# Kernel tuning notes

Hardware: AMD Instinct MI355X
Metric: run time of the kernel (lower is better)

## Reference

```python
import jax, jax.numpy as jnp
import numpy as np

EPSILON = 1e-4
MAX_ITER = 10


def setup_inputs() -> dict:
    key = jax.random.key(0)
    k1, k2, k3 = jax.random.split(key, 3)
    B, N, M = 64, 1024, 1024
    s = jax.random.uniform(k1, (B, N, M), dtype=jnp.float32)
    nrows = jax.random.randint(k2, (B,), 0, N, dtype=jnp.int32)
    ncols = jax.random.randint(k3, (B,), 0, M, dtype=jnp.int32)
    return {"s": s, "nrows": nrows, "ncols": ncols}


def reference(s, nrows, ncols):
    # s: [B, N, M]; nrows/ncols: [B] valid row/col counts per sample.
    B, N, M = s.shape
    row_mask = jnp.arange(N, dtype=nrows.dtype)[None, :] < nrows[:, None]  # [B, N]
    col_mask = jnp.arange(M, dtype=ncols.dtype)[None, :] < ncols[:, None]  # [B, M]
    mask = row_mask[:, :, None] & col_mask[:, None, :]  # [B, N, M]

    s = s + EPSILON
    for i in range(MAX_ITER):
        # i even -> column normalization (sum over dim 1); i odd -> row normalization (sum over dim 2)
        axis = 2 if i % 2 == 1 else 1
        ssum = jnp.sum(s, axis=axis, keepdims=True)
        tmp = jnp.where(mask, 1.0 / ssum, jnp.zeros((), dtype=s.dtype))
        s = s * tmp
    return s
```

## Files before the change

kernel.cpp:

```cpp
#include <hip/hip_runtime.h>

#define EPS 1e-4f

constexpr int Bn = 64;
constexpr int Nn = 1024;
constexpr int Mn = 1024;
constexpr int NSPLIT = 16;
constexpr int CHUNK  = Nn / NSPLIT;
constexpr int SLOT0  = 2 * NSPLIT;
constexpr int SLOT1  = 64;

__device__ __forceinline__ unsigned pk2(float a, float b) {
    unsigned ua = __float_as_uint(a); ua = (ua + 0x7fffu + ((ua >> 16) & 1u)) >> 16;
    unsigned ub = __float_as_uint(b); ub = (ub + 0x7fffu + ((ub >> 16) & 1u)) >> 16;
    return ua | (ub << 16);
}
__device__ __forceinline__ float lo16(unsigned v) { return __uint_as_float(v << 16); }
__device__ __forceinline__ float hi16(unsigned v) { return __uint_as_float(v & 0xffff0000u); }

__global__ __launch_bounds__(256) void fuse0_kernel(
        const float* __restrict__ s, unsigned short* __restrict__ sc,
        float* __restrict__ p) {
    const int b = blockIdx.x, sp = blockIdx.y;
    const int t = threadIdx.x, half = t >> 7, tc = t & 127;
    float acc[8];
    #pragma unroll
    for (int k = 0; k < 8; ++k) acc[k] = 0.f;
    for (int j = 0; j < CHUNK; j += 2) {
        const int n = sp * CHUNK + j + half;
        const size_t roff = ((size_t)b * Nn + n) * Mn;
        const float4* src = reinterpret_cast<const float4*>(s + roff) + 2 * tc;
        float4 v0 = src[0], v1 = src[1];
        v0.x += EPS; v0.y += EPS; v0.z += EPS; v0.w += EPS;
        v1.x += EPS; v1.y += EPS; v1.z += EPS; v1.w += EPS;
        acc[0] += v0.x; acc[1] += v0.y; acc[2] += v0.z; acc[3] += v0.w;
        acc[4] += v1.x; acc[5] += v1.y; acc[6] += v1.z; acc[7] += v1.w;
        uint4 w = { pk2(v0.x, v0.y), pk2(v0.z, v0.w),
                    pk2(v1.x, v1.y), pk2(v1.z, v1.w) };
        reinterpret_cast<uint4*>(sc + roff)[tc] = w;
    }
    float* pp = p + ((size_t)(b * SLOT1 + sp * 2 + half)) * Mn + tc * 8;
    float4 o0 = {acc[0], acc[1], acc[2], acc[3]};
    float4 o1 = {acc[4], acc[5], acc[6], acc[7]};
    *reinterpret_cast<float4*>(pp)     = o0;
    *reinterpret_cast<float4*>(pp + 4) = o1;
}

__global__ __launch_bounds__(256) void col_final_kernel(
        const float* __restrict__ p, const int* __restrict__ ncols,
        float* __restrict__ c, int slots) {
    const int b = blockIdx.x;
    const int m0 = threadIdx.x << 2;
    float sx = 0.f, sy = 0.f, sz = 0.f, sw = 0.f;
    for (int k = 0; k < slots; ++k) {
        float4 v = *reinterpret_cast<const float4*>(
            p + ((size_t)(b * SLOT1 + k)) * Mn + m0);
        sx += v.x; sy += v.y; sz += v.z; sw += v.w;
    }
    const int nc = ncols[b];
    float4 o;
    o.x = (m0 + 0 < nc && sx > 0.f) ? 1.f / sx : 0.f;
    o.y = (m0 + 1 < nc && sy > 0.f) ? 1.f / sy : 0.f;
    o.z = (m0 + 2 < nc && sz > 0.f) ? 1.f / sz : 0.f;
    o.w = (m0 + 3 < nc && sw > 0.f) ? 1.f / sw : 0.f;
    *reinterpret_cast<float4*>(c + (size_t)b * Mn + m0) = o;
}

__global__ __launch_bounds__(256) void rowcol_kernel(
        const unsigned short* __restrict__ sc, const float* __restrict__ c,
        const int* __restrict__ nrows, float* __restrict__ p) {
    const int b = blockIdx.x;
    const int t = threadIdx.x, w = t >> 6, l = t & 63;
    const int n0 = blockIdx.y * 64 + w * 16;
    const float4* cb = reinterpret_cast<const float4*>(c + (size_t)b * Mn);
    const float4 c0 = cb[2 * l], c1 = cb[2 * l + 1];
    const float4 c2 = cb[128 + 2 * l], c3 = cb[128 + 2 * l + 1];
    const int nr = nrows[b];
    float acc[16];
    #pragma unroll
    for (int k = 0; k < 16; ++k) acc[k] = 0.f;
    for (int j = 0; j < 16; ++j) {
        const int n = n0 + j;
        const uint4* row = reinterpret_cast<const uint4*>(sc + ((size_t)b * Nn + n) * Mn);
        uint4 a = row[l], d = row[64 + l];
        const float v0 = lo16(a.x), v1 = hi16(a.x), v2 = lo16(a.y), v3 = hi16(a.y);
        const float v4 = lo16(a.z), v5 = hi16(a.z), v6 = lo16(a.w), v7 = hi16(a.w);
        const float v8 = lo16(d.x), v9 = hi16(d.x), v10 = lo16(d.y), v11 = hi16(d.y);
        const float v12 = lo16(d.z), v13 = hi16(d.z), v14 = lo16(d.w), v15 = hi16(d.w);
        float part = v0 * c0.x + v1 * c0.y + v2 * c0.z + v3 * c0.w
                   + v4 * c1.x + v5 * c1.y + v6 * c1.z + v7 * c1.w
                   + v8 * c2.x + v9 * c2.y + v10 * c2.z + v11 * c2.w
                   + v12 * c3.x + v13 * c3.y + v14 * c3.z + v15 * c3.w;
        #pragma unroll
        for (int off = 1; off < 64; off <<= 1) part += __shfl_xor(part, off, 64);
        const float rv = (n < nr && part > 0.f) ? 1.f / part : 0.f;
        acc[0]  += v0 * rv;  acc[1]  += v1 * rv;  acc[2]  += v2 * rv;  acc[3]  += v3 * rv;
        acc[4]  += v4 * rv;  acc[5]  += v5 * rv;  acc[6]  += v6 * rv;  acc[7]  += v7 * rv;
        acc[8]  += v8 * rv;  acc[9]  += v9 * rv;  acc[10] += v10 * rv; acc[11] += v11 * rv;
        acc[12] += v12 * rv; acc[13] += v13 * rv; acc[14] += v14 * rv; acc[15] += v15 * rv;
    }
    float* pp = p + ((size_t)(b * SLOT1) + blockIdx.y * 4 + w) * Mn;
    float4 o;
    o = {acc[0], acc[1], acc[2], acc[3]};     *reinterpret_cast<float4*>(pp + 8 * l)           = o;
    o = {acc[4], acc[5], acc[6], acc[7]};     *reinterpret_cast<float4*>(pp + 8 * l + 4)       = o;
    o = {acc[8], acc[9], acc[10], acc[11]};   *reinterpret_cast<float4*>(pp + 512 + 8 * l)     = o;
    o = {acc[12], acc[13], acc[14], acc[15]}; *reinterpret_cast<float4*>(pp + 512 + 8 * l + 4) = o;
}

__global__ __launch_bounds__(256) void final_kernel(
        const float* __restrict__ s, const float* __restrict__ c,
        const int* __restrict__ nrows, float* __restrict__ out) {
    const int b = blockIdx.x;
    const int t = threadIdx.x, w = t >> 6, l = t & 63;
    const int n0 = blockIdx.y * 32 + w * 8;
    const float4* cb = reinterpret_cast<const float4*>(c + (size_t)b * Mn);
    float4 cc[4];
    #pragma unroll
    for (int k = 0; k < 4; ++k) cc[k] = cb[64 * k + l];
    const int nr = nrows[b];
    for (int j = 0; j < 8; ++j) {
        const int n = n0 + j;
        const size_t roff = ((size_t)b * Nn + n) * Mn;
        const float4* row = reinterpret_cast<const float4*>(s + roff);
        float4 a[4];
        float part = 0.f;
        #pragma unroll
        for (int k = 0; k < 4; ++k) {
            a[k] = row[64 * k + l];
            a[k].x += EPS; a[k].y += EPS; a[k].z += EPS; a[k].w += EPS;
            part += a[k].x * cc[k].x + a[k].y * cc[k].y
                  + a[k].z * cc[k].z + a[k].w * cc[k].w;
        }
        #pragma unroll
        for (int off = 1; off < 64; off <<= 1) part += __shfl_xor(part, off, 64);
        const float rv = (n < nr && part > 0.f) ? 1.f / part : 0.f;
        float4* orow = reinterpret_cast<float4*>(out + roff);
        #pragma unroll
        for (int k = 0; k < 4; ++k) {
            float4 o;
            o.x = a[k].x * cc[k].x * rv;
            o.y = a[k].y * cc[k].y * rv;
            o.z = a[k].z * cc[k].z * rv;
            o.w = a[k].w * cc[k].w * rv;
            orow[64 * k + l] = o;
        }
    }
}

extern "C" void kernel_launch(void* const* d_in, const int* in_sizes, int n_in,
                              void* d_out, int out_size, void* d_ws, size_t ws_size,
                              hipStream_t stream) {
    const float* s     = (const float*)d_in[0];
    const int*   nrows = (const int*)d_in[1];
    const int*   ncols = (const int*)d_in[2];
    float* out = (float*)d_out;

    unsigned short* sc = (unsigned short*)d_ws;
    float* p = (float*)(sc + (size_t)Bn * Nn * Mn);
    float* c = p + (size_t)Bn * SLOT1 * Mn;

    fuse0_kernel<<<dim3(Bn, NSPLIT), 256, 0, stream>>>(s, sc, p);
    col_final_kernel<<<Bn, 256, 0, stream>>>(p, ncols, c, SLOT0);
    for (int it = 0; it < 4; ++it) {
        rowcol_kernel<<<dim3(Bn, Nn / 64), 256, 0, stream>>>(sc, c, nrows, p);
        col_final_kernel<<<Bn, 256, 0, stream>>>(p, ncols, c, SLOT1);
    }
    final_kernel<<<dim3(Bn, Nn / 32), 256, 0, stream>>>(s, c, nrows, out);
}
```

Before: 714.5 us.

## Switch scratch copy to fp16, reduce partials in LDS, add nontemporal loads and stores

The compressed scratch copy of the matrix changes from bf16 to fp16, and fuse0 and rowcol now reduce their per-wave column partials through shared memory before writing. This cuts the number of partial slots from 64 to 16, and col_final is spread over more blocks with fewer loads. rowcol processes two rows per iteration for more independent work per loop, and the fp32 input and output streams use nontemporal loads and stores to avoid polluting the cache. The fp16 conversion changes rounding behaviour and adds a few cvt instructions, and the extra LDS reductions add a barrier per block.

After: 634.4 us. -11.2%, faster.

```diff
diff --git a/kernel.cpp b/kernel.cpp
--- a/kernel.cpp
+++ b/kernel.cpp
@@ -7,20 +7,28 @@
 constexpr int Mn = 1024;
 constexpr int NSPLIT = 16;
 constexpr int CHUNK  = Nn / NSPLIT;
-constexpr int SLOT0  = 2 * NSPLIT;
-constexpr int SLOT1  = 64;
-
-__device__ __forceinline__ unsigned pk2(float a, float b) {
-    unsigned ua = __float_as_uint(a); ua = (ua + 0x7fffu + ((ua >> 16) & 1u)) >> 16;
-    unsigned ub = __float_as_uint(b); ub = (ub + 0x7fffu + ((ub >> 16) & 1u)) >> 16;
-    return ua | (ub << 16);
-}
-__device__ __forceinline__ float lo16(unsigned v) { return __uint_as_float(v << 16); }
-__device__ __forceinline__ float hi16(unsigned v) { return __uint_as_float(v & 0xffff0000u); }
+constexpr int SLOT   = 16;
+
+typedef float f32x4 __attribute__((ext_vector_type(4)));
+
+__device__ __forceinline__ unsigned pkh2(float a, float b) {
+    union { _Float16 h; unsigned short u; } ta, tb;
+    ta.h = (_Float16)a; tb.h = (_Float16)b;
+    return (unsigned)ta.u | ((unsigned)tb.u << 16);
+}
+__device__ __forceinline__ float lo16(unsigned v) {
+    union { unsigned short u; _Float16 h; } t; t.u = (unsigned short)(v & 0xffffu);
+    return (float)t.h;
+}
+__device__ __forceinline__ float hi16(unsigned v) {
+    union { unsigned short u; _Float16 h; } t; t.u = (unsigned short)(v >> 16);
+    return (float)t.h;
+}
 
 __global__ __launch_bounds__(256) void fuse0_kernel(
         const float* __restrict__ s, unsigned short* __restrict__ sc,
         float* __restrict__ p) {
+    __shared__ float4 red[256];
     const int b = blockIdx.x, sp = blockIdx.y;
     const int t = threadIdx.x, half = t >> 7, tc = t & 127;
     float acc[8];
@@ -29,46 +37,47 @@
     for (int j = 0; j < CHUNK; j += 2) {
         const int n = sp * CHUNK + j + half;
         const size_t roff = ((size_t)b * Nn + n) * Mn;
-        const float4* src = reinterpret_cast<const float4*>(s + roff) + 2 * tc;
-        float4 v0 = src[0], v1 = src[1];
-        v0.x += EPS; v0.y += EPS; v0.z += EPS; v0.w += EPS;
-        v1.x += EPS; v1.y += EPS; v1.z += EPS; v1.w += EPS;
+        const f32x4* src = reinterpret_cast<const f32x4*>(s + roff) + 2 * tc;
+        f32x4 v0 = __builtin_nontemporal_load(src);
+        f32x4 v1 = __builtin_nontemporal_load(src + 1);
+        v0 += EPS; v1 += EPS;
         acc[0] += v0.x; acc[1] += v0.y; acc[2] += v0.z; acc[3] += v0.w;
         acc[4] += v1.x; acc[5] += v1.y; acc[6] += v1.z; acc[7] += v1.w;
-        uint4 w = { pk2(v0.x, v0.y), pk2(v0.z, v0.w),
-                    pk2(v1.x, v1.y), pk2(v1.z, v1.w) };
-        reinterpret_cast<uint4*>(sc + roff)[tc] = w;
-    }
-    float* pp = p + ((size_t)(b * SLOT1 + sp * 2 + half)) * Mn + tc * 8;
-    float4 o0 = {acc[0], acc[1], acc[2], acc[3]};
-    float4 o1 = {acc[4], acc[5], acc[6], acc[7]};
-    *reinterpret_cast<float4*>(pp)     = o0;
-    *reinterpret_cast<float4*>(pp + 4) = o1;
+        uint4 wpk = { pkh2(v0.x, v0.y), pkh2(v0.z, v0.w),
+                      pkh2(v1.x, v1.y), pkh2(v1.z, v1.w) };
+        reinterpret_cast<uint4*>(sc + roff)[tc] = wpk;
+    }
+    if (half) {
+        red[tc * 2]     = make_float4(acc[0], acc[1], acc[2], acc[3]);
+        red[tc * 2 + 1] = make_float4(acc[4], acc[5], acc[6], acc[7]);
+    }
+    __syncthreads();
+    if (!half) {
+        const float4 r0 = red[tc * 2], r1 = red[tc * 2 + 1];
+        float* pp = p + ((size_t)(b * SLOT + sp)) * Mn + tc * 8;
+        float4 o0 = {acc[0] + r0.x, acc[1] + r0.y, acc[2] + r0.z, acc[3] + r0.w};
+        float4 o1 = {acc[4] + r1.x, acc[5] + r1.y, acc[6] + r1.z, acc[7] + r1.w};
+        *reinterpret_cast<float4*>(pp)     = o0;
+        *reinterpret_cast<float4*>(pp + 4) = o1;
+    }
 }
 
 __global__ __launch_bounds__(256) void col_final_kernel(
         const float* __restrict__ p, const int* __restrict__ ncols,
-        float* __restrict__ c, int slots) {
+        float* __restrict__ c) {
     const int b = blockIdx.x;
-    const int m0 = threadIdx.x << 2;
-    float sx = 0.f, sy = 0.f, sz = 0.f, sw = 0.f;
-    for (int k = 0; k < slots; ++k) {
-        float4 v = *reinterpret_cast<const float4*>(
-            p + ((size_t)(b * SLOT1 + k)) * Mn + m0);
-        sx += v.x; sy += v.y; sz += v.z; sw += v.w;
-    }
-    const int nc = ncols[b];
-    float4 o;
-    o.x = (m0 + 0 < nc && sx > 0.f) ? 1.f / sx : 0.f;
-    o.y = (m0 + 1 < nc && sy > 0.f) ? 1.f / sy : 0.f;
-    o.z = (m0 + 2 < nc && sz > 0.f) ? 1.f / sz : 0.f;
-    o.w = (m0 + 3 < nc && sw > 0.f) ? 1.f / sw : 0.f;
-    *reinterpret_cast<float4*>(c + (size_t)b * Mn + m0) = o;
+    const int m = blockIdx.y * 256 + threadIdx.x;
+    float sum = 0.f;
+    #pragma unroll
+    for (int k = 0; k < SLOT; ++k)
+        sum += p[((size_t)(b * SLOT + k)) * Mn + m];
+    c[(size_t)b * Mn + m] = (m < ncols[b] && sum > 0.f) ? 1.f / sum : 0.f;
 }
 
 __global__ __launch_bounds__(256) void rowcol_kernel(
         const unsigned short* __restrict__ sc, const float* __restrict__ c,
         const int* __restrict__ nrows, float* __restrict__ p) {
+    __shared__ float4 red[4][256];
     const int b = blockIdx.x;
     const int t = threadIdx.x, w = t >> 6, l = t & 63;
     const int n0 = blockIdx.y * 64 + w * 16;
@@ -79,32 +88,54 @@
     float acc[16];
     #pragma unroll
     for (int k = 0; k < 16; ++k) acc[k] = 0.f;
-    for (int j = 0; j < 16; ++j) {
+    const uint4* base = reinterpret_cast<const uint4*>(sc + ((size_t)b * Nn + n0) * Mn);
+    for (int j = 0; j < 16; j += 2) {
+        const uint4* r0 = base + (size_t)j * 128;
+        const uint4 a0 = r0[l],       d0 = r0[64 + l];
+        const uint4 a1 = r0[128 + l], d1 = r0[192 + l];
+        const float x0 = lo16(a0.x),  x1 = hi16(a0.x),  x2 = lo16(a0.y),  x3 = hi16(a0.y);
+        const float x4 = lo16(a0.z),  x5 = hi16(a0.z),  x6 = lo16(a0.w),  x7 = hi16(a0.w);
+        const float x8 = lo16(d0.x),  x9 = hi16(d0.x),  x10 = lo16(d0.y), x11 = hi16(d0.y);
+        const float x12 = lo16(d0.z), x13 = hi16(d0.z), x14 = lo16(d0.w), x15 = hi16(d0.w);
+        const float y0 = lo16(a1.x),  y1 = hi16(a1.x),  y2 = lo16(a1.y),  y3 = hi16(a1.y);
+        const float y4 = lo16(a1.z),  y5 = hi16(a1.z),  y6 = lo16(a1.w),  y7 = hi16(a1.w);
+        const float y8 = lo16(d1.x),  y9 = hi16(d1.x),  y10 = lo16(d1.y), y11 = hi16(d1.y);
+        const float y12 = lo16(d1.z), y13 = hi16(d1.z), y14 = lo16(d1.w), y15 = hi16(d1.w);
+        float part0 = x0 * c0.x + x1 * c0.y + x2 * c0.z + x3 * c0.w
+                    + x4 * c1.x + x5 * c1.y + x6 * c1.z + x7 * c1.w
+                    + x8 * c2.x + x9 * c2.y + x10 * c2.z + x11 * c2.w
+                    + x12 * c3.x + x13 * c3.y + x14 * c3.z + x15 * c3.w;
+        float part1 = y0 * c0.x + y1 * c0.y + y2 * c0.z + y3 * c0.w
+                    + y4 * c1.x + y5 * c1.y + y6 * c1.z + y7 * c1.w
+                    + y8 * c2.x + y9 * c2.y + y10 * c2.z + y11 * c2.w
+                    + y12 * c3.x + y13 * c3.y + y14 * c3.z + y15 * c3.w;
+        #pragma unroll
+        for (int off = 1; off < 64; off <<= 1) {
+            part0 += __shfl_xor(part0, off, 64);
+            part1 += __shfl_xor(part1, off, 64);
+        }
         const int n = n0 + j;
-        const uint4* row = reinterpret_cast<const uint4*>(sc + ((size_t)b * Nn + n) * Mn);
-        uint4 a = row[l], d = row[64 + l];
-        const float v0 = lo16(a.x), v1 = hi16(a.x), v2 = lo16(a.y), v3 = hi16(a.y);
-        const float v4 = lo16(a.z), v5 = hi16(a.z), v6 = lo16(a.w), v7 = hi16(a.w);
-        const float v8 = lo16(d.x), v9 = hi16(d.x), v10 = lo16(d.y), v11 = hi16(d.y);
-        const float v12 = lo16(d.z), v13 = hi16(d.z), v14 = lo16(d.w), v15 = hi16(d.w);
-        float part = v0 * c0.x + v1 * c0.y + v2 * c0.z + v3 * c0.w
-                   + v4 * c1.x + v5 * c1.y + v6 * c1.z + v7 * c1.w
-                   + v8 * c2.x + v9 * c2.y + v10 * c2.z + v11 * c2.w
-                   + v12 * c3.x + v13 * c3.y + v14 * c3.z + v15 * c3.w;
-        #pragma unroll
-        for (int off = 1; off < 64; off <<= 1) part += __shfl_xor(part, off, 64);
-        const float rv = (n < nr && part > 0.f) ? 1.f / part : 0.f;
-        acc[0]  += v0 * rv;  acc[1]  += v1 * rv;  acc[2]  += v2 * rv;  acc[3]  += v3 * rv;
-        acc[4]  += v4 * rv;  acc[5]  += v5 * rv;  acc[6]  += v6 * rv;  acc[7]  += v7 * rv;
-        acc[8]  += v8 * rv;  acc[9]  += v9 * rv;  acc[10] += v10 * rv; acc[11] += v11 * rv;
-        acc[12] += v12 * rv; acc[13] += v13 * rv; acc[14] += v14 * rv; acc[15] += v15 * rv;
-    }
-    float* pp = p + ((size_t)(b * SLOT1) + blockIdx.y * 4 + w) * Mn;
-    float4 o;
-    o = {acc[0], acc[1], acc[2], acc[3]};     *reinterpret_cast<float4*>(pp + 8 * l)           = o;
-    o = {acc[4], acc[5], acc[6], acc[7]};     *reinterpret_cast<float4*>(pp + 8 * l + 4)       = o;
-    o = {acc[8], acc[9], acc[10], acc[11]};   *reinterpret_cast<float4*>(pp + 512 + 8 * l)     = o;
-    o = {acc[12], acc[13], acc[14], acc[15]}; *reinterpret_cast<float4*>(pp + 512 + 8 * l + 4) = o;
+        const float rv0 = (n < nr && part0 > 0.f) ? 1.f / part0 : 0.f;
+        const float rv1 = (n + 1 < nr && part1 > 0.f) ? 1.f / part1 : 0.f;
+        acc[0]  += x0 * rv0 + y0 * rv1;   acc[1]  += x1 * rv0 + y1 * rv1;
+        acc[2]  += x2 * rv0 + y2 * rv1;   acc[3]  += x3 * rv0 + y3 * rv1;
+        acc[4]  += x4 * rv0 + y4 * rv1;   acc[5]  += x5 * rv0 + y5 * rv1;
+        acc[6]  += x6 * rv0 + y6 * rv1;   acc[7]  += x7 * rv0 + y7 * rv1;
+        acc[8]  += x8 * rv0 + y8 * rv1;   acc[9]  += x9 * rv0 + y9 * rv1;
+        acc[10] += x10 * rv0 + y10 * rv1; acc[11] += x11 * rv0 + y11 * rv1;
+        acc[12] += x12 * rv0 + y12 * rv1; acc[13] += x13 * rv0 + y13 * rv1;
+        acc[14] += x14 * rv0 + y14 * rv1; acc[15] += x15 * rv0 + y15 * rv1;
+    }
+    red[w][2 * l]       = make_float4(acc[0], acc[1], acc[2], acc[3]);
+    red[w][2 * l + 1]   = make_float4(acc[4], acc[5], acc[6], acc[7]);
+    red[w][128 + 2 * l] = make_float4(acc[8], acc[9], acc[10], acc[11]);
+    red[w][129 + 2 * l] = make_float4(acc[12], acc[13], acc[14], acc[15]);
+    __syncthreads();
+    const float4 r0 = red[0][t], r1 = red[1][t], r2 = red[2][t], r3 = red[3][t];
+    float4 o = { r0.x + r1.x + r2.x + r3.x, r0.y + r1.y + r2.y + r3.y,
+                 r0.z + r1.z + r2.z + r3.z, r0.w + r1.w + r2.w + r3.w };
+    float* pp = p + ((size_t)(b * SLOT) + blockIdx.y) * Mn;
+    reinterpret_cast<float4*>(pp)[t] = o;
 }
 
 __global__ __launch_bounds__(256) void final_kernel(
@@ -121,28 +152,28 @@
     for (int j = 0; j < 8; ++j) {
         const int n = n0 + j;
         const size_t roff = ((size_t)b * Nn + n) * Mn;
-        const float4* row = reinterpret_cast<const float4*>(s + roff);
-        float4 a[4];
+        const f32x4* row = reinterpret_cast<const f32x4*>(s + roff);
+        f32x4 a[4];
         float part = 0.f;
         #pragma unroll
         for (int k = 0; k < 4; ++k) {
-            a[k] = row[64 * k + l];
-            a[k].x += EPS; a[k].y += EPS; a[k].z += EPS; a[k].w += EPS;
+            a[k] = __builtin_nontemporal_load(row + 64 * k + l);
+            a[k] += EPS;
             part += a[k].x * cc[k].x + a[k].y * cc[k].y
                   + a[k].z * cc[k].z + a[k].w * cc[k].w;
         }
         #pragma unroll
         for (int off = 1; off < 64; off <<= 1) part += __shfl_xor(part, off, 64);
         const float rv = (n < nr && part > 0.f) ? 1.f / part : 0.f;
-        float4* orow = reinterpret_cast<float4*>(out + roff);
+        f32x4* orow = reinterpret_cast<f32x4*>(out + roff);
         #pragma unroll
         for (int k = 0; k < 4; ++k) {
-            float4 o;
+            f32x4 o;
             o.x = a[k].x * cc[k].x * rv;
             o.y = a[k].y * cc[k].y * rv;
             o.z = a[k].z * cc[k].z * rv;
             o.w = a[k].w * cc[k].w * rv;
-            orow[64 * k + l] = o;
+            __builtin_nontemporal_store(o, orow + 64 * k + l);
         }
     }
 }
@@ -157,13 +188,13 @@
 
     unsigned short* sc = (unsigned short*)d_ws;
     float* p = (float*)(sc + (size_t)Bn * Nn * Mn);
-    float* c = p + (size_t)Bn * SLOT1 * Mn;
+    float* c = p + (size_t)Bn * SLOT * Mn;
 
     fuse0_kernel<<<dim3(Bn, NSPLIT), 256, 0, stream>>>(s, sc, p);
-    col_final_kernel<<<Bn, 256, 0, stream>>>(p, ncols, c, SLOT0);
+    col_final_kernel<<<dim3(Bn, Mn / 256), 256, 0, stream>>>(p, ncols, c);
     for (int it = 0; it < 4; ++it) {
         rowcol_kernel<<<dim3(Bn, Nn / 64), 256, 0, stream>>>(sc, c, nrows, p);
-        col_final_kernel<<<Bn, 256, 0, stream>>>(p, ncols, c, SLOT1);
+        col_final_kernel<<<dim3(Bn, Mn / 256), 256, 0, stream>>>(p, ncols, c);
     }
     final_kernel<<<dim3(Bn, Nn / 32), 256, 0, stream>>>(s, c, nrows, out);
 }
```
